# Kernel tuning notes

Measured on AMD Instinct MI355X. Metric: run time of the kernel, lower is better.

Reference implementation:

```python
import jax, jax.numpy as jnp
import numpy as np

EPS = 1e-5

def conv2d(x, w, stride, pad):
    return jax.lax.conv_general_dilated(
        x, w, window_strides=(stride, stride),
        padding=[(pad, pad), (pad, pad)],
        dimension_numbers=('NCHW', 'OIHW', 'NCHW'))

def batchnorm(x, gamma, beta, mean, var):
    # inference-mode BN over channel dim of NCHW
    inv = jax.lax.rsqrt(var + EPS)
    return (x - mean[None, :, None, None]) * (inv * gamma)[None, :, None, None] + beta[None, :, None, None]

def rational(x, num, den):
    # Rational activation, version A, degrees (5,4):
    #   P(x) = num0 + num1*x + ... + num5*x^5  (Horner)
    #   Q(x) = 1 + sum_{j=1..4} |den_{j-1}| * |x|^j
    p = num[5]
    for i in range(4, -1, -1):
        p = p * x + num[i]
    xa = jnp.abs(x)
    q = jnp.ones_like(x)
    pw = xa
    for j in range(4):
        q = q + jnp.abs(den[j]) * pw
        pw = pw * xa
    return p / q

def multi_variant_rationals(out, num_r, den_r, num_g, den_g, num_b, den_b):
    # channels 0::3 -> r, 1::3 -> g, 2::3 -> b, then re-interleave
    B, C, H, W = out.shape
    o = out.reshape(B, C // 3, 3, H, W)  # channel c = 3*j + k
    r = rational(o[:, :, 0], num_r, den_r)
    g = rational(o[:, :, 1], num_g, den_g)
    b = rational(o[:, :, 2], num_b, den_b)
    return jnp.stack([r, g, b], axis=2).reshape(B, C, H, W)

def setup_inputs() -> dict:
    key = jax.random.key(0)
    ks = jax.random.split(key, 12)
    B, Cin, Cout, H, W = 64, 96, 192, 56, 56
    inp = {
        'x': jax.random.normal(ks[0], (B, Cin, H, W), jnp.float32),
        'w1': jax.random.normal(ks[1], (Cout, Cin, 3, 3), jnp.float32) * 0.05,
        'gamma1': jnp.ones((Cout,), jnp.float32),
        'beta1': jnp.zeros((Cout,), jnp.float32),
        'mean1': jnp.zeros((Cout,), jnp.float32),
        'var1': jnp.ones((Cout,), jnp.float32),
        'num_r': jax.random.normal(ks[2], (6,), jnp.float32) * 0.3,
        'den_r': jax.random.normal(ks[3], (4,), jnp.float32) * 0.3,
        'num_g': jax.random.normal(ks[4], (6,), jnp.float32) * 0.3,
        'den_g': jax.random.normal(ks[5], (4,), jnp.float32) * 0.3,
        'num_b': jax.random.normal(ks[6], (6,), jnp.float32) * 0.3,
        'den_b': jax.random.normal(ks[7], (4,), jnp.float32) * 0.3,
        'w2': jax.random.normal(ks[8], (Cout, Cout, 3, 3), jnp.float32) * 0.05,
        'gamma2': jnp.ones((Cout,), jnp.float32),
        'beta2': jnp.zeros((Cout,), jnp.float32),
        'mean2': jnp.zeros((Cout,), jnp.float32),
        'var2': jnp.ones((Cout,), jnp.float32),
        'ws': jax.random.normal(ks[9], (Cout, Cin, 1, 1), jnp.float32) * 0.05,
        'gammas': jnp.ones((Cout,), jnp.float32),
        'betas': jnp.zeros((Cout,), jnp.float32),
        'means': jnp.zeros((Cout,), jnp.float32),
        'vars_': jnp.ones((Cout,), jnp.float32),
    }
    return inp

def reference(x, w1, gamma1, beta1, mean1, var1,
              num_r, den_r, num_g, den_g, num_b, den_b,
              w2, gamma2, beta2, mean2, var2,
              ws, gammas, betas, means, vars_):
    STRIDE = 2
    out = batchnorm(conv2d(x, w1, STRIDE, 1), gamma1, beta1, mean1, var1)
    out = multi_variant_rationals(out, num_r, den_r, num_g, den_g, num_b, den_b)
    out = batchnorm(conv2d(out, w2, 1, 1), gamma2, beta2, mean2, var2)
    shortcut = batchnorm(conv2d(x, ws, STRIDE, 0), gammas, betas, means, vars_)
    out = out + shortcut
    out = multi_variant_rationals(out, num_r, den_r, num_g, den_g, num_b, den_b)
    return out
```

## Files before the change

### kernel.cpp

```cpp
#include <hip/hip_runtime.h>

#define EPSBN  1e-5f
#define NBLK   392

#define W1B_OFF 0u
#define W2B_OFF 331776u
#define WSB_OFF 995328u
#define CS_OFF  1044480u
#define XT_OFF  1048320u
#define ACT_OFF 39583488u

typedef __attribute__((ext_vector_type(8))) short bf16x8;
typedef __attribute__((ext_vector_type(4))) short bf16x4;
typedef __attribute__((ext_vector_type(4))) float f32x4;

__device__ __forceinline__ short f2bf(float f) {
    unsigned u = __float_as_uint(f);
    u += 0x7fffu + ((u >> 16) & 1u);
    return (short)(u >> 16);
}

__device__ __forceinline__ void gload16(const short* g, short* l) {
    __builtin_amdgcn_global_load_lds(
        (const __attribute__((address_space(1))) void*)g,
        (__attribute__((address_space(3))) void*)l, 16, 0, 0);
}

__device__ __forceinline__ float rational_eval(float v, const float* nm, const float* dn) {
    float p = nm[5];
    p = p * v + nm[4];
    p = p * v + nm[3];
    p = p * v + nm[2];
    p = p * v + nm[1];
    p = p * v + nm[0];
    float xa = fabsf(v);
    float q = 1.0f;
    float pw = xa;
    q += dn[0] * pw; pw *= xa;
    q += dn[1] * pw; pw *= xa;
    q += dn[2] * pw; pw *= xa;
    q += dn[3] * pw;
    float inv = __builtin_amdgcn_rcpf(q);
    inv = inv * (2.0f - q * inv);
    return p * inv;
}

__device__ __forceinline__ void sel_coeffs(int v, const float cnm[3][6], const float cdn[3][4],
                                           float nm[6], float dn[4]) {
#pragma unroll
    for (int i = 0; i < 6; i++) nm[i] = (v == 0) ? cnm[0][i] : ((v == 1) ? cnm[1][i] : cnm[2][i]);
#pragma unroll
    for (int i = 0; i < 4; i++) dn[i] = (v == 0) ? cdn[0][i] : ((v == 1) ? cdn[1][i] : cdn[2][i]);
}

extern "C" __global__ void prep_scales_kernel(
    const float* g1, const float* b1, const float* m1, const float* v1,
    const float* g2, const float* b2, const float* m2, const float* v2,
    const float* gs, const float* bs, const float* ms, const float* vs,
    float* cs)
{
    int i = threadIdx.x;
    if (i < 192) {
        float a1 = g1[i] * rsqrtf(v1[i] + EPSBN);
        float a2 = g2[i] * rsqrtf(v2[i] + EPSBN);
        float a3 = gs[i] * rsqrtf(vs[i] + EPSBN);
        cs[i]       = a1;
        cs[192 + i] = a2;
        cs[384 + i] = a3;
        cs[576 + i] = b1[i] - m1[i] * a1;
        cs[768 + i] = (b2[i] - m2[i] * a2) + (bs[i] - ms[i] * a3);
    }
}

extern "C" __global__ void prep_w_kernel(const float* __restrict__ w, const float* __restrict__ s,
                                         short* __restrict__ wb, int CI_src, int CI_dst, int KP, int total)
{
    int i = blockIdx.x * 256 + threadIdx.x;
    if (i >= total) return;
    int co = i / (CI_dst * KP);
    int r  = i - co * CI_dst * KP;
    int kpos = r / CI_dst;
    int ci = r - kpos * CI_dst;
    wb[i] = (ci < CI_src) ? f2bf(w[(co * CI_src + ci) * KP + kpos] * s[co]) : (short)0;
}

extern "C" __global__ void ring_zero_kernel(short* __restrict__ buf, int H, int C, int total)
{
    int ring = 2 * H + 2 * (H - 2);
    int i = blockIdx.x * 256 + threadIdx.x;
    if (i >= total) return;
    int c = i % C;
    int t = i / C;
    int rp = t % ring;
    int n = t / ring;
    int h, w;
    if (rp < H)           { h = 0;          w = rp; }
    else if (rp < 2 * H)  { h = H - 1;      w = rp - H; }
    else { int k = rp - 2 * H; h = (k >> 1) + 1; w = (k & 1) ? (H - 1) : 0; }
    buf[((n * H + h) * H + w) * C + c] = 0;
}

extern "C" __global__ __launch_bounds__(256)
void xpose_kernel(const float* __restrict__ x, short* __restrict__ xt)
{
    __shared__ float t[96 * 57];
    int b = blockIdx.x;
    int n = b / 56, h = b - n * 56;
    const float* src = x + n * (96 * 3136) + h * 56;
    for (int i = threadIdx.x; i < 96 * 28; i += 256) {
        int c = i / 28, w2 = i - c * 28;
        float2 v = *(const float2*)&src[c * 3136 + w2 * 2];
        t[c * 57 + w2 * 2]     = v.x;
        t[c * 57 + w2 * 2 + 1] = v.y;
    }
    __syncthreads();
    unsigned* dst = (unsigned*)(xt + (n * 56 + h) * 56 * 96);
    for (int i = threadIdx.x; i < 56 * 48; i += 256) {
        int w = i / 96 * 0 + i / 48, cp = i - (i / 48) * 48;
        unsigned lo = (unsigned short)f2bf(t[(2 * cp) * 57 + w]);
        unsigned hi = (unsigned short)f2bf(t[(2 * cp + 1) * 57 + w]);
        dst[w * 48 + cp] = lo | (hi << 16);
    }
}

extern "C" __global__ __launch_bounds__(512, 4)
void convA_kernel(const short* __restrict__ xt,
                  const short* __restrict__ w1b,
                  const short* __restrict__ zbuf,
                  const float* __restrict__ bias1,
                  const float* __restrict__ num_r, const float* __restrict__ den_r,
                  const float* __restrict__ num_g, const float* __restrict__ den_g,
                  const float* __restrict__ num_b, const float* __restrict__ den_b,
                  short* __restrict__ act)
{
    __shared__ short lA[2][192 * 32];
    __shared__ short lB[2][128 * 32];

    const int tid  = threadIdx.x;
    const int lane = tid & 63;
    const int wave = tid >> 6;
    const int wm = wave >> 1, wn = wave & 1;
    const int lbid = (blockIdx.x & 7) * 49 + (blockIdx.x >> 3);
    const int p0   = lbid * 128;

    const int sA = (((tid & 3) ^ ((tid >> 3) & 3))) * 8;
    const int r1 = tid >> 2;
    const int aw1a = r1 * 864 + sA;
    const int aw1b = (128 + r1) * 864 + sA;

    int xb0; bool top, left;
    {
        int p = p0 + r1;
        int n = p / 784; int pr = p - n * 784;
        int oh = pr / 28; int ow = pr - oh * 28;
        xb0 = ((n * 56 + 2 * oh) * 56 + 2 * ow) * 96 + sA;
        top = (oh == 0); left = (ow == 0);
    }

    const int l15 = lane & 15, ksl = lane >> 4;
    int ard[3], brd[4];
#pragma unroll
    for (int m = 0; m < 3; ++m) {
        int row = wm * 48 + m * 16 + l15;
        ard[m] = row * 32 + ((ksl ^ ((row >> 1) & 3)) << 3);
    }
#pragma unroll
    for (int n = 0; n < 4; ++n) {
        int row = wn * 64 + n * 16 + l15;
        brd[n] = row * 32 + ((ksl ^ ((row >> 1) & 3)) << 3);
    }

    auto stage = [&](int buf, int t) {
        int kpos = t / 3, cb = t - 3 * kpos;
        int kh = kpos / 3, kw = kpos - 3 * kh;
        gload16(&w1b[aw1a + t * 32], &lA[buf][wave * 512]);
        if (tid < 256) gload16(&w1b[aw1b + t * 32], &lA[buf][4096 + wave * 512]);
        int bko = ((kh - 1) * 56 + (kw - 1)) * 96 + cb * 32;
        const short* src = (((kh == 0) && top) || ((kw == 0) && left)) ? zbuf : &xt[xb0 + bko];
        gload16(src, &lB[buf][wave * 512]);
    };

    f32x4 acc[3][4];
#pragma unroll
    for (int m = 0; m < 3; m++)
#pragma unroll
        for (int n = 0; n < 4; n++) acc[m][n] = (f32x4){0.f, 0.f, 0.f, 0.f};

    stage(0, 0);
    int cur = 0;
    for (int t = 0; t < 27; ++t) {
        __syncthreads();
        if (t + 1 < 27) stage(cur ^ 1, t + 1);
        bf16x8 af[3];
#pragma unroll
        for (int m = 0; m < 3; ++m) af[m] = *(const bf16x8*)&lA[cur][ard[m]];
#pragma unroll
        for (int n = 0; n < 4; ++n) {
            bf16x8 bv = *(const bf16x8*)&lB[cur][brd[n]];
#pragma unroll
            for (int m = 0; m < 3; ++m)
                acc[m][n] = __builtin_amdgcn_mfma_f32_16x16x32_bf16(af[m], bv, acc[m][n], 0, 0, 0);
        }
        cur ^= 1;
    }

    float cnm[3][6], cdn[3][4];
#pragma unroll
    for (int i = 0; i < 6; i++) { cnm[0][i] = num_r[i]; cnm[1][i] = num_g[i]; cnm[2][i] = num_b[i]; }
#pragma unroll
    for (int i = 0; i < 4; i++) { cdn[0][i] = fabsf(den_r[i]); cdn[1][i] = fabsf(den_g[i]); cdn[2][i] = fabsf(den_b[i]); }

    int abase[4];
#pragma unroll
    for (int n = 0; n < 4; ++n) {
        int pp = p0 + wn * 64 + n * 16 + l15;
        int n2 = pp / 784; int r2 = pp - n2 * 784;
        int oh2 = r2 / 28; int ow2 = r2 - oh2 * 28;
        abase[n] = ((n2 * 30 + oh2 + 1) * 30 + ow2 + 1) * 192;
    }
#pragma unroll
    for (int m = 0; m < 3; ++m) {
        int cob = wm * 48 + m * 16 + (ksl << 2);
        float res[4][4];
#pragma unroll
        for (int r = 0; r < 4; ++r) {
            float nm[6], dn[4];
            sel_coeffs((cob + r) % 3, cnm, cdn, nm, dn);
            float bv = bias1[cob + r];
#pragma unroll
            for (int n = 0; n < 4; ++n)
                res[n][r] = rational_eval(acc[m][n][r] + bv, nm, dn);
        }
#pragma unroll
        for (int n = 0; n < 4; ++n) {
            bf16x4 pk;
#pragma unroll
            for (int r = 0; r < 4; ++r) pk[r] = f2bf(res[n][r]);
            *(bf16x4*)&act[abase[n] + cob] = pk;
        }
    }
}

extern "C" __global__ __launch_bounds__(512, 4)
void convB_kernel(const short* __restrict__ act,
                  const short* __restrict__ xt,
                  const short* __restrict__ w2b,
                  const short* __restrict__ wsb,
                  const float* __restrict__ bias2s,
                  const float* __restrict__ num_r, const float* __restrict__ den_r,
                  const float* __restrict__ num_g, const float* __restrict__ den_g,
                  const float* __restrict__ num_b, const float* __restrict__ den_b,
                  float* __restrict__ outp)
{
    __shared__ short lA[2][192 * 64];
    __shared__ short lB[2][128 * 64];

    const int tid  = threadIdx.x;
    const int lane = tid & 63;
    const int wave = tid >> 6;
    const int wm = wave >> 1, wn = wave & 1;
    const int lbid = (blockIdx.x & 7) * 49 + (blockIdx.x >> 3);
    const int p0   = lbid * 128;

    const int s8 = (((tid & 7) ^ ((tid >> 3) & 7))) * 8;
    const int rA = tid >> 3;

    int awW[3], awS[3];
#pragma unroll
    for (int c = 0; c < 3; ++c) {
        int row = c * 64 + rA;
        awW[c] = row * 1728 + s8;
        awS[c] = row * 128 + s8;
    }
    int abB[2], xcB[2];
#pragma unroll
    for (int c = 0; c < 2; ++c) {
        int p = p0 + c * 64 + rA;
        int n = p / 784; int pr = p - n * 784;
        int oh = pr / 28; int ow = pr - oh * 28;
        abB[c] = ((n * 30 + oh) * 30 + ow) * 192 + s8;
        xcB[c] = ((n * 56 + 2 * oh) * 56 + 2 * ow) * 96 + s8;
    }

    const int l15 = lane & 15, ksl = lane >> 4;
    int ard[2][3], brd[2][4];
#pragma unroll
    for (int kk = 0; kk < 2; ++kk) {
#pragma unroll
        for (int m = 0; m < 3; ++m) {
            int row = wm * 48 + m * 16 + l15;
            ard[kk][m] = row * 64 + ((((kk << 2) | ksl) ^ (row & 7)) << 3);
        }
#pragma unroll
        for (int n = 0; n < 4; ++n) {
            int row = wn * 64 + n * 16 + l15;
            brd[kk][n] = row * 64 + ((((kk << 2) | ksl) ^ (row & 7)) << 3);
        }
    }

    auto stage = [&](int buf, int t) {
        if (t < 2) {
#pragma unroll
            for (int c = 0; c < 3; ++c)
                gload16(&wsb[awS[c] + t * 64], &lA[buf][c * 4096 + wave * 512]);
#pragma unroll
            for (int c = 0; c < 2; ++c)
                gload16(&xt[xcB[c] + t * 64], &lB[buf][c * 4096 + wave * 512]);
        } else {
            int u = t - 2;
            int kpos = u / 3, cb = u - 3 * kpos;
            int kh = kpos / 3, kw = kpos - 3 * kh;
            int bko = (kh * 30 + kw) * 192 + cb * 64;
#pragma unroll
            for (int c = 0; c < 3; ++c)
                gload16(&w2b[awW[c] + u * 64], &lA[buf][c * 4096 + wave * 512]);
#pragma unroll
            for (int c = 0; c < 2; ++c)
                gload16(&act[abB[c] + bko], &lB[buf][c * 4096 + wave * 512]);
        }
    };

    f32x4 acc[3][4];
#pragma unroll
    for (int m = 0; m < 3; m++)
#pragma unroll
        for (int n = 0; n < 4; n++) acc[m][n] = (f32x4){0.f, 0.f, 0.f, 0.f};

    stage(0, 0);
    int cur = 0;
    for (int t = 0; t < 29; ++t) {
        __syncthreads();
        if (t + 1 < 29) stage(cur ^ 1, t + 1);
#pragma unroll
        for (int kk = 0; kk < 2; ++kk) {
            bf16x8 af[3];
#pragma unroll
            for (int m = 0; m < 3; ++m) af[m] = *(const bf16x8*)&lA[cur][ard[kk][m]];
#pragma unroll
            for (int n = 0; n < 4; ++n) {
                bf16x8 bv = *(const bf16x8*)&lB[cur][brd[kk][n]];
#pragma unroll
                for (int m = 0; m < 3; ++m)
                    acc[m][n] = __builtin_amdgcn_mfma_f32_16x16x32_bf16(af[m], bv, acc[m][n], 0, 0, 0);
            }
        }
        cur ^= 1;
    }

    float cnm[3][6], cdn[3][4];
#pragma unroll
    for (int i = 0; i < 6; i++) { cnm[0][i] = num_r[i]; cnm[1][i] = num_g[i]; cnm[2][i] = num_b[i]; }
#pragma unroll
    for (int i = 0; i < 4; i++) { cdn[0][i] = fabsf(den_r[i]); cdn[1][i] = fabsf(den_g[i]); cdn[2][i] = fabsf(den_b[i]); }

    int obase[4];
#pragma unroll
    for (int n = 0; n < 4; ++n) {
        int pp = p0 + wn * 64 + n * 16 + l15;
        int n2 = pp / 784; int r2 = pp - n2 * 784;
        int oh2 = r2 / 28; int ow2 = r2 - oh2 * 28;
        obase[n] = n2 * (192 * 784) + oh2 * 28 + ow2;
    }
#pragma unroll
    for (int m = 0; m < 3; ++m) {
        int cob = wm * 48 + m * 16 + (ksl << 2);
#pragma unroll
        for (int r = 0; r < 4; ++r) {
            float nm[6], dn[4];
            sel_coeffs((cob + r) % 3, cnm, cdn, nm, dn);
            float bv = bias2s[cob + r];
#pragma unroll
            for (int n = 0; n < 4; ++n) {
                int idx = obase[n] + (cob + r) * 784;
                outp[idx] = rational_eval(acc[m][n][r] + bv, nm, dn);
            }
        }
    }
}

extern "C" void kernel_launch(void* const* d_in, const int* in_sizes, int n_in,
                              void* d_out, int out_size, void* d_ws, size_t ws_size,
                              hipStream_t stream)
{
    const float* x      = (const float*)d_in[0];
    const float* w1     = (const float*)d_in[1];
    const float* gamma1 = (const float*)d_in[2];
    const float* beta1  = (const float*)d_in[3];
    const float* mean1  = (const float*)d_in[4];
    const float* var1   = (const float*)d_in[5];
    const float* num_r  = (const float*)d_in[6];
    const float* den_r  = (const float*)d_in[7];
    const float* num_g  = (const float*)d_in[8];
    const float* den_g  = (const float*)d_in[9];
    const float* num_b  = (const float*)d_in[10];
    const float* den_b  = (const float*)d_in[11];
    const float* w2     = (const float*)d_in[12];
    const float* gamma2 = (const float*)d_in[13];
    const float* beta2  = (const float*)d_in[14];
    const float* mean2  = (const float*)d_in[15];
    const float* var2   = (const float*)d_in[16];
    const float* wsc    = (const float*)d_in[17];
    const float* gammas = (const float*)d_in[18];
    const float* betas  = (const float*)d_in[19];
    const float* means  = (const float*)d_in[20];
    const float* vars_  = (const float*)d_in[21];

    char* base = (char*)d_ws;
    short* w1b  = (short*)(base + W1B_OFF);
    short* w2b  = (short*)(base + W2B_OFF);
    short* wsb  = (short*)(base + WSB_OFF);
    float* cs   = (float*)(base + CS_OFF);
    short* xt   = (short*)(base + XT_OFF);
    short* act  = (short*)(base + ACT_OFF);
    float* outp = (float*)d_out;

    float* bias1  = cs + 576;
    float* bias2s = cs + 768;
    const short* zbuf = wsb + 96;

    prep_scales_kernel<<<1, 256, 0, stream>>>(gamma1, beta1, mean1, var1,
                                              gamma2, beta2, mean2, var2,
                                              gammas, betas, means, vars_, cs);

    prep_w_kernel<<<(192 * 96 * 9 + 255) / 256, 256, 0, stream>>>(w1, cs, w1b, 96, 96, 9, 192 * 96 * 9);
    prep_w_kernel<<<(192 * 192 * 9 + 255) / 256, 256, 0, stream>>>(w2, cs + 192, w2b, 192, 192, 9, 192 * 192 * 9);
    prep_w_kernel<<<(192 * 128 + 255) / 256, 256, 0, stream>>>(wsc, cs + 384, wsb, 96, 128, 1, 192 * 128);

    {
        int tot_a = 64 * (2 * 30 + 2 * 28) * 192;
        ring_zero_kernel<<<(tot_a + 255) / 256, 256, 0, stream>>>(act, 30, 192, tot_a);
    }

    xpose_kernel<<<64 * 56, 256, 0, stream>>>(x, xt);

    convA_kernel<<<NBLK, 512, 0, stream>>>(xt, w1b, zbuf, bias1,
                                           num_r, den_r, num_g, den_g, num_b, den_b,
                                           act);

    convB_kernel<<<NBLK, 512, 0, stream>>>(act, xt, w2b, wsb, bias2s,
                                           num_r, den_r, num_g, den_g, num_b, den_b,
                                           outp);
}
```

Baseline: 143.8 us.

## Merge prep kernels, triple-buffer convA pipeline, and widen transpose stores

Folds the scale, weight-prep and ring-zero kernels into one launch to cut launch overhead. The convA K-loop moves from double to triple buffering, using explicit vmcnt waits and raw s_barrier so two stages stay in flight, and the loop is fully unrolled. The transpose kernel now writes four bf16 channels per store instead of two, and ring zeroing uses 4-wide stores. The cost is more LDS per block, which may reduce occupancy, and hand-written waitcnt logic that depends on the exact count of outstanding loads per wave.

```diff
diff --git a/kernel.cpp b/kernel.cpp
--- a/kernel.cpp
+++ b/kernel.cpp
@@ -1,7 +1,9 @@
 #include <hip/hip_runtime.h>
 
 #define EPSBN  1e-5f
-#define NBLK   392
+#define NBLK_A 392
+#define NBLK_B 392
+#define PSTR   196
 
 #define W1B_OFF 0u
 #define W2B_OFF 331776u
@@ -13,6 +15,8 @@
 typedef __attribute__((ext_vector_type(8))) short bf16x8;
 typedef __attribute__((ext_vector_type(4))) short bf16x4;
 typedef __attribute__((ext_vector_type(4))) float f32x4;
+
+#define WAITV(N) asm volatile("s_waitcnt vmcnt(" #N ")" ::: "memory")
 
 __device__ __forceinline__ short f2bf(float f) {
     unsigned u = __float_as_uint(f);
@@ -53,51 +57,58 @@
     for (int i = 0; i < 4; i++) dn[i] = (v == 0) ? cdn[0][i] : ((v == 1) ? cdn[1][i] : cdn[2][i]);
 }
 
-extern "C" __global__ void prep_scales_kernel(
+extern "C" __global__ void prep_all_kernel(
+    const float* __restrict__ w1, const float* __restrict__ w2, const float* __restrict__ wsc,
     const float* g1, const float* b1, const float* m1, const float* v1,
     const float* g2, const float* b2, const float* m2, const float* v2,
     const float* gs, const float* bs, const float* ms, const float* vs,
-    float* cs)
+    short* __restrict__ w1b, short* __restrict__ w2b, short* __restrict__ wsb,
+    float* __restrict__ cs, short* __restrict__ act)
 {
-    int i = threadIdx.x;
-    if (i < 192) {
-        float a1 = g1[i] * rsqrtf(v1[i] + EPSBN);
-        float a2 = g2[i] * rsqrtf(v2[i] + EPSBN);
-        float a3 = gs[i] * rsqrtf(vs[i] + EPSBN);
-        cs[i]       = a1;
-        cs[192 + i] = a2;
-        cs[384 + i] = a3;
-        cs[576 + i] = b1[i] - m1[i] * a1;
-        cs[768 + i] = (b2[i] - m2[i] * a2) + (bs[i] - ms[i] * a3);
-    }
-}
-
-extern "C" __global__ void prep_w_kernel(const float* __restrict__ w, const float* __restrict__ s,
-                                         short* __restrict__ wb, int CI_src, int CI_dst, int KP, int total)
-{
-    int i = blockIdx.x * 256 + threadIdx.x;
-    if (i >= total) return;
-    int co = i / (CI_dst * KP);
-    int r  = i - co * CI_dst * KP;
-    int kpos = r / CI_dst;
-    int ci = r - kpos * CI_dst;
-    wb[i] = (ci < CI_src) ? f2bf(w[(co * CI_src + ci) * KP + kpos] * s[co]) : (short)0;
-}
-
-extern "C" __global__ void ring_zero_kernel(short* __restrict__ buf, int H, int C, int total)
-{
-    int ring = 2 * H + 2 * (H - 2);
-    int i = blockIdx.x * 256 + threadIdx.x;
-    if (i >= total) return;
-    int c = i % C;
-    int t = i / C;
-    int rp = t % ring;
-    int n = t / ring;
-    int h, w;
-    if (rp < H)           { h = 0;          w = rp; }
-    else if (rp < 2 * H)  { h = H - 1;      w = rp - H; }
-    else { int k = rp - 2 * H; h = (k >> 1) + 1; w = (k & 1) ? (H - 1) : 0; }
-    buf[((n * H + h) * H + w) * C + c] = 0;
+    int blk = blockIdx.x;
+    if (blk < 1296) {
+        int i = blk * 256 + threadIdx.x;
+        int co = i / 1728;
+        int r  = i - co * 1728;
+        int kpos = r / 192;
+        int ci = r - kpos * 192;
+        float a = g2[co] * rsqrtf(v2[co] + EPSBN);
+        w2b[i] = f2bf(w2[(co * 192 + ci) * 9 + kpos] * a);
+    } else if (blk < 1944) {
+        int i = (blk - 1296) * 256 + threadIdx.x;
+        int co = i / 864;
+        int r  = i - co * 864;
+        int kpos = r / 96;
+        int ci = r - kpos * 96;
+        float a = g1[co] * rsqrtf(v1[co] + EPSBN);
+        w1b[i] = f2bf(w1[(co * 96 + ci) * 9 + kpos] * a);
+    } else if (blk < 2040) {
+        int i = (blk - 1944) * 256 + threadIdx.x;
+        int co = i >> 7;
+        int ci = i & 127;
+        float a = gs[co] * rsqrtf(vs[co] + EPSBN);
+        wsb[i] = (ci < 96) ? f2bf(wsc[co * 96 + ci] * a) : (short)0;
+    } else if (blk < 3432) {
+        int i = (blk - 2040) * 256 + threadIdx.x;
+        int c4 = i % 48;
+        int t = i / 48;
+        int rp = t % 116;
+        int n = t / 116;
+        int h, w;
+        if (rp < 30)      { h = 0;  w = rp; }
+        else if (rp < 60) { h = 29; w = rp - 30; }
+        else { int k = rp - 60; h = (k >> 1) + 1; w = (k & 1) ? 29 : 0; }
+        *(bf16x4*)&act[((n * 30 + h) * 30 + w) * 192 + c4 * 4] = (bf16x4)(short)0;
+    } else {
+        int i = threadIdx.x;
+        if (i < 192) {
+            float a1 = g1[i] * rsqrtf(v1[i] + EPSBN);
+            float a2 = g2[i] * rsqrtf(v2[i] + EPSBN);
+            float a3 = gs[i] * rsqrtf(vs[i] + EPSBN);
+            cs[576 + i] = b1[i] - m1[i] * a1;
+            cs[768 + i] = (b2[i] - m2[i] * a2) + (bs[i] - ms[i] * a3);
+        }
+    }
 }
 
 extern "C" __global__ __launch_bounds__(256)
@@ -115,11 +126,14 @@
     }
     __syncthreads();
     unsigned* dst = (unsigned*)(xt + (n * 56 + h) * 56 * 96);
-    for (int i = threadIdx.x; i < 56 * 48; i += 256) {
-        int w = i / 96 * 0 + i / 48, cp = i - (i / 48) * 48;
-        unsigned lo = (unsigned short)f2bf(t[(2 * cp) * 57 + w]);
-        unsigned hi = (unsigned short)f2bf(t[(2 * cp + 1) * 57 + w]);
-        dst[w * 48 + cp] = lo | (hi << 16);
+    for (int i = threadIdx.x; i < 56 * 24; i += 256) {
+        int w = i / 24, cp2 = i - (i / 24) * 24;
+        unsigned u0 = (unsigned short)f2bf(t[(4 * cp2 + 0) * 57 + w]);
+        unsigned u1 = (unsigned short)f2bf(t[(4 * cp2 + 1) * 57 + w]);
+        unsigned u2 = (unsigned short)f2bf(t[(4 * cp2 + 2) * 57 + w]);
+        unsigned u3 = (unsigned short)f2bf(t[(4 * cp2 + 3) * 57 + w]);
+        uint2 pk; pk.x = u0 | (u1 << 16); pk.y = u2 | (u3 << 16);
+        *(uint2*)&dst[w * 48 + cp2 * 2] = pk;
     }
 }
 
@@ -133,8 +147,8 @@
                   const float* __restrict__ num_b, const float* __restrict__ den_b,
                   short* __restrict__ act)
 {
-    __shared__ short lA[2][192 * 32];
-    __shared__ short lB[2][128 * 32];
+    __shared__ short lA[3][192 * 32];
+    __shared__ short lB[3][128 * 32];
 
     const int tid  = threadIdx.x;
     const int lane = tid & 63;
@@ -187,10 +201,14 @@
         for (int n = 0; n < 4; n++) acc[m][n] = (f32x4){0.f, 0.f, 0.f, 0.f};
 
     stage(0, 0);
-    int cur = 0;
+    stage(1, 1);
+    WAITV(0);
+    __builtin_amdgcn_s_barrier();
+
+#pragma unroll
     for (int t = 0; t < 27; ++t) {
-        __syncthreads();
-        if (t + 1 < 27) stage(cur ^ 1, t + 1);
+        const int cur = t % 3;
+        if (t + 2 < 27) stage((t + 2) % 3, t + 2);
         bf16x8 af[3];
 #pragma unroll
         for (int m = 0; m < 3; ++m) af[m] = *(const bf16x8*)&lA[cur][ard[m]];
@@ -201,7 +219,14 @@
             for (int m = 0; m < 3; ++m)
                 acc[m][n] = __builtin_amdgcn_mfma_f32_16x16x32_bf16(af[m], bv, acc[m][n], 0, 0, 0);
         }
-        cur ^= 1;
+        if (t + 1 < 27) {
+            if (t + 2 < 27) {
+                if (wave < 4) { WAITV(3); } else { WAITV(2); }
+            } else {
+                WAITV(0);
+            }
+            __builtin_amdgcn_s_barrier();
+        }
     }
 
     float cnm[3][6], cdn[3][4];
@@ -418,26 +443,19 @@
     float* bias2s = cs + 768;
     const short* zbuf = wsb + 96;
 
-    prep_scales_kernel<<<1, 256, 0, stream>>>(gamma1, beta1, mean1, var1,
+    prep_all_kernel<<<3433, 256, 0, stream>>>(w1, w2, wsc,
+                                              gamma1, beta1, mean1, var1,
                                               gamma2, beta2, mean2, var2,
-                                              gammas, betas, means, vars_, cs);
-
-    prep_w_kernel<<<(192 * 96 * 9 + 255) / 256, 256, 0, stream>>>(w1, cs, w1b, 96, 96, 9, 192 * 96 * 9);
-    prep_w_kernel<<<(192 * 192 * 9 + 255) / 256, 256, 0, stream>>>(w2, cs + 192, w2b, 192, 192, 9, 192 * 192 * 9);
-    prep_w_kernel<<<(192 * 128 + 255) / 256, 256, 0, stream>>>(wsc, cs + 384, wsb, 96, 128, 1, 192 * 128);
-
-    {
-        int tot_a = 64 * (2 * 30 + 2 * 28) * 192;
-        ring_zero_kernel<<<(tot_a + 255) / 256, 256, 0, stream>>>(act, 30, 192, tot_a);
-    }
+                                              gammas, betas, means, vars_,
+                                              w1b, w2b, wsb, cs, act);
 
     xpose_kernel<<<64 * 56, 256, 0, stream>>>(x, xt);
 
-    convA_kernel<<<NBLK, 512, 0, stream>>>(xt, w1b, zbuf, bias1,
-                                           num_r, den_r, num_g, den_g, num_b, den_b,
-                                           act);
-
-    convB_kernel<<<NBLK, 512, 0, stream>>>(act, xt, w2b, wsb, bias2s,
-                                           num_r, den_r, num_g, den_g, num_b, den_b,
-                                           outp);
-}
+    convA_kernel<<<NBLK_A, 512, 0, stream>>>(xt, w1b, zbuf, bias1,
+                                             num_r, den_r, num_g, den_g, num_b, den_b,
+                                             act);
+
+    convB_kernel<<<NBLK_B, 512, 0, stream>>>(act, xt, w2b, wsb, bias2s,
+                                             num_r, den_r, num_g, den_g, num_b, den_b,
+                                             outp);
+}
```

Result: faster. 130.7 us (-9.1%).
